# Performance work log

Hardware: AMD Instinct MI355X
Metric: run time of the kernel (lower is better)

The kernel has to match this reference:

```python
import jax, jax.numpy as jnp
import numpy as np

N_NODES = 100000
D = 128
N_EDGES = 640000


def _spmm(edge_index, w, x, n):
    # out[i] = sum over edges (i<-j): w * x[j]
    src, dst = edge_index[0], edge_index[1]
    return jax.ops.segment_sum(w[:, None] * x[dst], src, num_segments=n)


def setup_inputs() -> dict:
    key = jax.random.key(0)
    ks = jax.random.split(key, 8)
    inp = {
        "index_vectors": jax.random.normal(ks[0], (N_NODES, D), dtype=jnp.float32),
        "edge_index1": jax.random.randint(ks[1], (2, N_EDGES), 0, N_NODES, dtype=jnp.int64),
        "w1": jnp.ones((N_EDGES,), dtype=jnp.float32),
        "edge_index2": jax.random.randint(ks[2], (2, N_EDGES), 0, N_NODES, dtype=jnp.int64),
        "w2": jnp.ones((N_EDGES,), dtype=jnp.float32),
        "edge_index3": jax.random.randint(ks[3], (2, N_EDGES), 0, N_NODES, dtype=jnp.int64),
        "w3": jnp.ones((N_EDGES,), dtype=jnp.float32),
        "zeroth": jax.random.uniform(ks[4], (1, 1), dtype=jnp.float32),
        "fst": jax.random.uniform(ks[5], (1, 1), dtype=jnp.float32),
        "snd": jax.random.uniform(ks[6], (1, 1), dtype=jnp.float32),
        "trd": jax.random.uniform(ks[7], (1, 1), dtype=jnp.float32),
    }
    return inp


def reference(index_vectors, edge_index1, w1, edge_index2, w2, edge_index3, w3,
              zeroth, fst, snd, trd):
    n = index_vectors.shape[0]
    # hop-1 context: A @ x
    fst_ctx = _spmm(edge_index1, w1, index_vectors, n)
    # hop-2 context: A^2 @ roll(x, 1, axis=1)   (permute_vecs=True)
    snd_ctx = _spmm(edge_index2, w2, jnp.roll(index_vectors, 1, axis=1), n)
    # hop-3 context: A^3 @ roll(x, 2, axis=1)
    trd_ctx = _spmm(edge_index3, w3, jnp.roll(index_vectors, 2, axis=1), n)

    # relu-normalized scalar order weights (get_orders)
    r0, r1, r2, r3 = (jax.nn.relu(zeroth), jax.nn.relu(fst),
                      jax.nn.relu(snd), jax.nn.relu(trd))
    tot = r0 + r1 + r2 + r3 + 1e-6
    r0, r1, r2, r3 = r0 / tot, r1 / tot, r2 / tot, r3 / tot

    # use_sign=False -> plain weighted combination
    return r0 * index_vectors + r1 * fst_ctx + r2 * snd_ctx + r3 * trd_ctx
```

## Files before the change

kernel.cpp:

```cpp
#include <hip/hip_runtime.h>

#define N_NODES 100000
#define D 128
#define N_EDGES 640000
#define TOT_EDGES (3 * N_EDGES)

#define NB   256
#define NPB  391
#define BCAP 9216
#define OVF_CAP 16384
#define EPB  3072
#define BINA_BLOCKS (TOT_EDGES / EPB)
#define EPT  (EPB / 256)
#define NKEY 2048

#define WS_OVFCNT 0
#define WS_BCUR   64
#define WS_BBASE  16448
#define WS_BNUM   17472
#define WS_OVF    18496
#define WS_TMP    280640
#define WS_FREC   19155008
#define WS_OFFS   34515008
#define WS_XB     34915016
#define WS_TOTAL_FAST 60515016

#ifndef __has_builtin
#define __has_builtin(x) 0
#endif
#if __has_builtin(__builtin_amdgcn_alignbit)
#define ALIGN16(hi, lo) __builtin_amdgcn_alignbit((hi), (lo), 16)
#else
#define ALIGN16(hi, lo) (((hi) << 16) | ((lo) >> 16))
#endif

__device__ __forceinline__ void load_r(const float* z0, const float* z1,
                                       const float* z2, const float* z3,
                                       float& r0, float& r1, float& r2, float& r3) {
    r0 = fmaxf(z0[0], 0.0f);
    r1 = fmaxf(z1[0], 0.0f);
    r2 = fmaxf(z2[0], 0.0f);
    r3 = fmaxf(z3[0], 0.0f);
    float inv = 1.0f / (r0 + r1 + r2 + r3 + 1e-6f);
    r0 *= inv; r1 *= inv; r2 *= inv; r3 *= inv;
}

__device__ __forceinline__ unsigned short bf16rn(float f) {
    unsigned int u = __float_as_uint(f);
    u += 0x7FFFu + ((u >> 16) & 1u);
    return (unsigned short)(u >> 16);
}

__global__ void cast_kernel(const float* __restrict__ x, ushort* __restrict__ xb) {
    int i = blockIdx.x * 256 + threadIdx.x;
    if (i >= N_NODES * D / 4) return;
    float4 v = ((const float4*)x)[i];
    ushort4 h;
    h.x = bf16rn(v.x); h.y = bf16rn(v.y); h.z = bf16rn(v.z); h.w = bf16rn(v.w);
    ((ushort4*)xb)[i] = h;
}

__global__ void binA_kernel(const int* __restrict__ ei1, const float* __restrict__ w1,
                            const int* __restrict__ ei2, const float* __restrict__ w2,
                            const int* __restrict__ ei3, const float* __restrict__ w3,
                            const float* __restrict__ z0, const float* __restrict__ z1,
                            const float* __restrict__ z2, const float* __restrict__ z3,
                            int* __restrict__ bcur, int* __restrict__ ovf_count,
                            int4* __restrict__ ovf, int2* __restrict__ tmp) {
    __shared__ int hist[NB];
    __shared__ int base[NB];
    int t = threadIdx.x;
    hist[t] = 0;
    __syncthreads();

    float r0, r1, r2, r3;
    load_r(z0, z1, z2, z3, r0, r1, r2, r3);

    int e0 = blockIdx.x * EPB;
    int rank[EPT];
    int bkt[EPT];
    int rxv[EPT];
    float scv[EPT];

#pragma unroll
    for (int k = 0; k < EPT; ++k) {
        int e = e0 + t + k * 256;
        int set = e / N_EDGES;
        int idx = e - set * N_EDGES;
        const int* ei;  const float* w;  float rk;
        if      (set == 0) { ei = ei1; w = w1; rk = r1; }
        else if (set == 1) { ei = ei2; w = w2; rk = r2; }
        else               { ei = ei3; w = w3; rk = r3; }
        int src = ei[idx];
        int dst = ei[N_EDGES + idx];
        int b = src / NPB;
        int local = src - b * NPB;
        bkt[k]  = b;
        rxv[k]  = dst | (set << 17) | (local << 19);
        scv[k]  = rk * w[idx];
        rank[k] = atomicAdd(&hist[b], 1);
    }
    __syncthreads();

    {
        int h = hist[t];
        base[t] = h ? atomicAdd(&bcur[t * 16], h) : 0;
    }
    __syncthreads();

#pragma unroll
    for (int k = 0; k < EPT; ++k) {
        int b = bkt[k];
        int pos = base[b] + rank[k];
        if (pos < BCAP) {
            tmp[(size_t)b * BCAP + pos] = make_int2(rxv[k], __float_as_int(scv[k]));
        } else {
            int o = atomicAdd(ovf_count, 1);
            int src = b * NPB + ((rxv[k] >> 19) & 0x1FF);
            if (o < OVF_CAP) ovf[o] = make_int4(src, rxv[k] & 0x7FFFF,
                                                __float_as_int(scv[k]), 0);
        }
    }
}

__global__ void scanB_kernel(const int* __restrict__ bcur,
                             int* __restrict__ bbase, int* __restrict__ bnum,
                             int* __restrict__ offsets) {
    __shared__ int s[NB];
    int t = threadIdx.x;
    int n = bcur[t * 16];
    if (n > BCAP) n = BCAP;
    bnum[t] = n;
    s[t] = n;
    __syncthreads();
    for (int off = 1; off < NB; off <<= 1) {
        int v = (t >= off) ? s[t - off] : 0;
        __syncthreads();
        s[t] += v;
        __syncthreads();
    }
    bbase[t] = s[t] - n;
    if (t == NB - 1) offsets[N_NODES] = s[t];
}

__global__ void binB_kernel(const int2* __restrict__ tmp,
                            const int* __restrict__ bbase, const int* __restrict__ bnum,
                            int2* __restrict__ frecs, int* __restrict__ offsets) {
    __shared__ int d[NKEY];
    __shared__ int ts[256];
    __shared__ int cur[NKEY];
    int b = blockIdx.x;
    int t = threadIdx.x;
    int n = bnum[b];
    int gbase = bbase[b];

    for (int i = t; i < NKEY; i += 256) d[i] = 0;
    __syncthreads();
    for (int i = t; i < n; i += 256) {
        int rx = tmp[(size_t)b * BCAP + i].x;
        int key = (((rx >> 19) & 0x1FF) << 2) | ((rx >> 17) & 3);
        atomicAdd(&d[key], 1);
    }
    __syncthreads();

    int loc[8];
    int tot = 0;
#pragma unroll
    for (int k = 0; k < 8; ++k) { loc[k] = tot; tot += d[8 * t + k]; }
    ts[t] = tot;
    __syncthreads();
    for (int off = 1; off < 256; off <<= 1) {
        int v = (t >= off) ? ts[t - off] : 0;
        __syncthreads();
        ts[t] += v;
        __syncthreads();
    }
    int tbase = ts[t] - tot;
#pragma unroll
    for (int k = 0; k < 8; ++k) cur[8 * t + k] = tbase + loc[k];
    __syncthreads();

    int node0 = b * NPB;
    for (int l = t; l < NPB; l += 256) {
        int node = node0 + l;
        if (node < N_NODES) offsets[node] = gbase + cur[l << 2];
    }
    __syncthreads();

    for (int i = t; i < n; i += 256) {
        int2 rec = tmp[(size_t)b * BCAP + i];
        int key = (((rec.x >> 19) & 0x1FF) << 2) | ((rec.x >> 17) & 3);
        int pos = atomicAdd(&cur[key], 1);
        frecs[gbase + pos] = make_int2(rec.x & 0x7FFFF, rec.y);
    }
}

#define GB_ACCUM(RX, RY)                                                       \
    {                                                                          \
        const uint4* rowp = (const uint4*)(xb + (size_t)((RX) & 0x1FFFF) * D); \
        uint4 v = rowp[l16];                                                   \
        int sh = ((RX) >> 17) & 3;                                             \
        float sc = __int_as_float(RY);                                         \
        unsigned int pw = (unsigned int)__shfl((int)v.w, prevq);               \
        unsigned int s1x = ALIGN16(v.x, pw);                                   \
        unsigned int s1y = ALIGN16(v.y, v.x);                                  \
        unsigned int s1z = ALIGN16(v.z, v.y);                                  \
        unsigned int s1w = ALIGN16(v.w, v.z);                                  \
        unsigned int u0 = (sh == 0) ? v.x : (sh == 1) ? s1x : pw;              \
        unsigned int u1 = (sh == 0) ? v.y : (sh == 1) ? s1y : v.x;             \
        unsigned int u2 = (sh == 0) ? v.z : (sh == 1) ? s1z : v.y;             \
        unsigned int u3 = (sh == 0) ? v.w : (sh == 1) ? s1w : v.z;             \
        acc0 += sc * __uint_as_float(u0 << 16);                                \
        acc1 += sc * __uint_as_float(u0 & 0xFFFF0000u);                        \
        acc2 += sc * __uint_as_float(u1 << 16);                                \
        acc3 += sc * __uint_as_float(u1 & 0xFFFF0000u);                        \
        acc4 += sc * __uint_as_float(u2 << 16);                                \
        acc5 += sc * __uint_as_float(u2 & 0xFFFF0000u);                        \
        acc6 += sc * __uint_as_float(u3 << 16);                                \
        acc7 += sc * __uint_as_float(u3 & 0xFFFF0000u);                        \
    }

__global__ void gatherb_kernel(const float* __restrict__ x,
                               const ushort* __restrict__ xb,
                               const int* __restrict__ offsets,
                               const int2* __restrict__ recs,
                               const float* __restrict__ z0, const float* __restrict__ z1,
                               const float* __restrict__ z2, const float* __restrict__ z3,
                               float* __restrict__ out) {
    int wid  = (blockIdx.x * blockDim.x + threadIdx.x) >> 6;
    int lane = threadIdx.x & 63;
    if (wid >= N_NODES) return;

    float r0, r1, r2, r3;
    load_r(z0, z1, z2, z3, r0, r1, r2, r3);

    int qt    = lane >> 4;
    int l16   = lane & 15;
    int prevq = (qt << 4) | ((l16 + 15) & 15);

    int beg = offsets[wid];
    int end = offsets[wid + 1];
    int count = end - beg;
    int cnt64 = (count < 64) ? count : 64;

    int mrx = 0, mry = 0;
    if (lane < cnt64) { int2 rec = recs[beg + lane]; mrx = rec.x; mry = rec.y; }

    float acc0 = 0.f, acc1 = 0.f, acc2 = 0.f, acc3 = 0.f;
    float acc4 = 0.f, acc5 = 0.f, acc6 = 0.f, acc7 = 0.f;

    for (int j = 0; j < cnt64; j += 4) {
        int srcl = j + qt;
        int rx = __shfl(mrx, srcl);
        int ry = __shfl(mry, srcl);
        GB_ACCUM(rx, ry)
    }
    for (int q = 64; q < count; q += 4) {
        int qq = q + qt;
        int rx = 0, ry = 0;
        if (qq < count) { int2 rec = recs[beg + qq]; rx = rec.x; ry = rec.y; }
        GB_ACCUM(rx, ry)
    }

    acc0 += __shfl_xor(acc0, 16); acc0 += __shfl_xor(acc0, 32);
    acc1 += __shfl_xor(acc1, 16); acc1 += __shfl_xor(acc1, 32);
    acc2 += __shfl_xor(acc2, 16); acc2 += __shfl_xor(acc2, 32);
    acc3 += __shfl_xor(acc3, 16); acc3 += __shfl_xor(acc3, 32);
    acc4 += __shfl_xor(acc4, 16); acc4 += __shfl_xor(acc4, 32);
    acc5 += __shfl_xor(acc5, 16); acc5 += __shfl_xor(acc5, 32);
    acc6 += __shfl_xor(acc6, 16); acc6 += __shfl_xor(acc6, 32);
    acc7 += __shfl_xor(acc7, 16); acc7 += __shfl_xor(acc7, 32);

    if (lane < 16) {
        const float4* xr = (const float4*)(x + (size_t)wid * D);
        float4 xlo = xr[2 * l16];
        float4 xhi = xr[2 * l16 + 1];
        float4 olo, ohi;
        olo.x = r0 * xlo.x + acc0;
        olo.y = r0 * xlo.y + acc1;
        olo.z = r0 * xlo.z + acc2;
        olo.w = r0 * xlo.w + acc3;
        ohi.x = r0 * xhi.x + acc4;
        ohi.y = r0 * xhi.y + acc5;
        ohi.z = r0 * xhi.z + acc6;
        ohi.w = r0 * xhi.w + acc7;
        float4* op = (float4*)(out + (size_t)wid * D);
        op[2 * l16]     = olo;
        op[2 * l16 + 1] = ohi;
    }
}

__global__ void ovf_kernel(const float* __restrict__ x,
                           const int* __restrict__ ovf_count,
                           const int4* __restrict__ ovf,
                           float* __restrict__ out) {
    int total_waves = (gridDim.x * blockDim.x) >> 6;
    int gw   = (blockIdx.x * blockDim.x + threadIdx.x) >> 6;
    int lane = threadIdx.x & 63;
    int n = *ovf_count;
    if (n > OVF_CAP) n = OVF_CAP;
    for (int r = gw; r < n; r += total_waves) {
        int4 rec = ovf[r];
        int src = rec.x;
        int dst = rec.y & 0x1FFFF;
        int sh  = (rec.y >> 17) & 3;
        float sc = __int_as_float(rec.z);
        const float* xr = x + (size_t)dst * D;
        float* orow = out + (size_t)src * D;
        int c0 = 2 * lane, c1 = 2 * lane + 1;
        atomicAdd(&orow[c0], sc * xr[(c0 - sh) & 127]);
        atomicAdd(&orow[c1], sc * xr[(c1 - sh) & 127]);
    }
}

#define SCAN_BLOCKS ((N_NODES + 255) / 256)
#define WS_COUNTS   0
#define WS_OFFSETS  400000
#define WS_CURSORS  800008
#define WS_BSUM     1200008
#define WS_BPRE     1201576
#define WS_RECS     1203144
#define WS_NEEDED_MID (WS_RECS + (size_t)TOT_EDGES * 8)

__global__ void hist_kernel(const int* __restrict__ ei1, const int* __restrict__ ei2,
                            const int* __restrict__ ei3, int* __restrict__ counts) {
    int e = blockIdx.x * blockDim.x + threadIdx.x;
    if (e >= TOT_EDGES) return;
    int set = e / N_EDGES;
    int idx = e - set * N_EDGES;
    const int* ei = (set == 0) ? ei1 : (set == 1) ? ei2 : ei3;
    atomicAdd(&counts[ei[idx]], 1);
}

__global__ void scan1_kernel(const int* __restrict__ counts,
                             int* __restrict__ offsets, int* __restrict__ bsum) {
    __shared__ int s[256];
    int t = threadIdx.x;
    int i = blockIdx.x * 256 + t;
    int v = (i < N_NODES) ? counts[i] : 0;
    s[t] = v;
    __syncthreads();
    for (int off = 1; off < 256; off <<= 1) {
        int u = (t >= off) ? s[t - off] : 0;
        __syncthreads();
        s[t] += u;
        __syncthreads();
    }
    if (i < N_NODES) offsets[i] = s[t] - v;
    if (t == 255) bsum[blockIdx.x] = s[255];
}

__global__ void scan2_kernel(const int* __restrict__ bsum, int* __restrict__ bpre) {
    __shared__ int s[512];
    int t = threadIdx.x;
    int v = (t < SCAN_BLOCKS) ? bsum[t] : 0;
    s[t] = v;
    __syncthreads();
    for (int off = 1; off < 512; off <<= 1) {
        int u = (t >= off) ? s[t - off] : 0;
        __syncthreads();
        s[t] += u;
        __syncthreads();
    }
    if (t < SCAN_BLOCKS) bpre[t] = s[t] - v;
}

__global__ void scan3_kernel(int* __restrict__ offsets, const int* __restrict__ bpre,
                             int* __restrict__ cursors) {
    int i = blockIdx.x * 256 + threadIdx.x;
    if (i < N_NODES) {
        int v = offsets[i] + bpre[blockIdx.x];
        offsets[i] = v;
        cursors[i] = v;
    }
    if (i == 0) offsets[N_NODES] = TOT_EDGES;
}

__global__ void fill_kernel(const int* __restrict__ ei1, const float* __restrict__ w1,
                            const int* __restrict__ ei2, const float* __restrict__ w2,
                            const int* __restrict__ ei3, const float* __restrict__ w3,
                            const float* __restrict__ z0, const float* __restrict__ z1,
                            const float* __restrict__ z2, const float* __restrict__ z3,
                            int* __restrict__ cursors, int2* __restrict__ recs) {
    int e = blockIdx.x * blockDim.x + threadIdx.x;
    if (e >= TOT_EDGES) return;
    int set = e / N_EDGES;
    int idx = e - set * N_EDGES;
    const int* ei;  const float* w;
    if      (set == 0) { ei = ei1; w = w1; }
    else if (set == 1) { ei = ei2; w = w2; }
    else               { ei = ei3; w = w3; }
    float r0, r1, r2, r3;
    load_r(z0, z1, z2, z3, r0, r1, r2, r3);
    float rk = (set == 0) ? r1 : (set == 1) ? r2 : r3;
    int src = ei[idx];
    int dst = ei[N_EDGES + idx];
    float scale = rk * w[idx];
    int pos = atomicAdd(&cursors[src], 1);
    recs[pos] = make_int2(dst | (set << 17), __float_as_int(scale));
}

__global__ void gatherd_kernel(const float* __restrict__ x,
                               const int* __restrict__ offsets,
                               const int2* __restrict__ recs,
                               const float* __restrict__ z0, const float* __restrict__ z1,
                               const float* __restrict__ z2, const float* __restrict__ z3,
                               float* __restrict__ out) {
    int wid  = (blockIdx.x * blockDim.x + threadIdx.x) >> 6;
    int lane = threadIdx.x & 63;
    if (wid >= N_NODES) return;
    float r0, r1, r2, r3;
    load_r(z0, z1, z2, z3, r0, r1, r2, r3);
    float2 xv = ((const float2*)(x + (size_t)wid * D))[lane];
    int beg = offsets[wid];
    int end = offsets[wid + 1];
    float2 a0 = {0.f, 0.f}, a1 = {0.f, 0.f}, a2 = {0.f, 0.f};
    for (int j = beg; j < end; ++j) {
        int2 rec = recs[j];
        float2 v = ((const float2*)(x + (size_t)(rec.x & 0x1FFFF) * D))[lane];
        int sh = (rec.x >> 17) & 3;
        float sc = __int_as_float(rec.y);
        if      (sh == 0) { a0.x += sc * v.x; a0.y += sc * v.y; }
        else if (sh == 1) { a1.x += sc * v.x; a1.y += sc * v.y; }
        else               { a2.x += sc * v.x; a2.y += sc * v.y; }
    }
    int prev = (lane + 63) & 63;
    float r1y = __shfl(a1.y, prev);
    float r2x = __shfl(a2.x, prev);
    float r2y = __shfl(a2.y, prev);
    float2 o;
    o.x = r0 * xv.x + a0.x + r1y  + r2x;
    o.y = r0 * xv.y + a0.y + a1.x + r2y;
    ((float2*)(out + (size_t)wid * D))[lane] = o;
}

extern "C" void kernel_launch(void* const* d_in, const int* in_sizes, int n_in,
                              void* d_out, int out_size, void* d_ws, size_t ws_size,
                              hipStream_t stream) {
    const float* x   = (const float*)d_in[0];
    const int*   ei1 = (const int*)  d_in[1];
    const float* w1  = (const float*)d_in[2];
    const int*   ei2 = (const int*)  d_in[3];
    const float* w2  = (const float*)d_in[4];
    const int*   ei3 = (const int*)  d_in[5];
    const float* w3  = (const float*)d_in[6];
    const float* z0  = (const float*)d_in[7];
    const float* z1  = (const float*)d_in[8];
    const float* z2  = (const float*)d_in[9];
    const float* z3  = (const float*)d_in[10];
    float* out = (float*)d_out;
    char* wsc = (char*)d_ws;

    if (ws_size >= WS_TOTAL_FAST) {
        int*    ovf_count = (int*)   (wsc + WS_OVFCNT);
        int*    bcur      = (int*)   (wsc + WS_BCUR);
        int*    bbase     = (int*)   (wsc + WS_BBASE);
        int*    bnum      = (int*)   (wsc + WS_BNUM);
        int4*   ovf       = (int4*)  (wsc + WS_OVF);
        int2*   tmp       = (int2*)  (wsc + WS_TMP);
        int2*   frecs     = (int2*)  (wsc + WS_FREC);
        int*    offsets   = (int*)   (wsc + WS_OFFS);
        ushort* xb        = (ushort*)(wsc + WS_XB);

        hipMemsetAsync(wsc, 0, WS_BBASE, stream);
        cast_kernel<<<(N_NODES * D / 4 + 255) / 256, 256, 0, stream>>>(x, xb);
        binA_kernel<<<BINA_BLOCKS, 256, 0, stream>>>(ei1, w1, ei2, w2, ei3, w3,
                                                     z0, z1, z2, z3,
                                                     bcur, ovf_count, ovf, tmp);
        scanB_kernel<<<1, NB, 0, stream>>>(bcur, bbase, bnum, offsets);
        binB_kernel<<<NB, 256, 0, stream>>>(tmp, bbase, bnum, frecs, offsets);
        gatherb_kernel<<<(N_NODES * 64 + 255) / 256, 256, 0, stream>>>(x, xb, offsets,
                                                                       frecs, z0, z1, z2, z3,
                                                                       out);
        ovf_kernel<<<128, 256, 0, stream>>>(x, ovf_count, ovf, out);
    } else {
        int*  counts  = (int*) (wsc + WS_COUNTS);
        int*  offsets = (int*) (wsc + WS_OFFSETS);
        int*  cursors = (int*) (wsc + WS_CURSORS);
        int*  bsum    = (int*) (wsc + WS_BSUM);
        int*  bpre    = (int*) (wsc + WS_BPRE);
        int2* recs    = (int2*)(wsc + WS_RECS);

        hipMemsetAsync(counts, 0, N_NODES * sizeof(int), stream);
        hist_kernel<<<TOT_EDGES / 256, 256, 0, stream>>>(ei1, ei2, ei3, counts);
        scan1_kernel<<<SCAN_BLOCKS, 256, 0, stream>>>(counts, offsets, bsum);
        scan2_kernel<<<1, 512, 0, stream>>>(bsum, bpre);
        scan3_kernel<<<SCAN_BLOCKS, 256, 0, stream>>>(offsets, bpre, cursors);
        fill_kernel<<<TOT_EDGES / 256, 256, 0, stream>>>(ei1, w1, ei2, w2, ei3, w3,
                                                         z0, z1, z2, z3, cursors, recs);
        gatherd_kernel<<<(N_NODES * 64 + 255) / 256, 256, 0, stream>>>(x, offsets, recs,
                                                                       z0, z1, z2, z3, out);
    }
}
```

Measured before the change: 280.3 us.

## Restructure edge binning into deterministic hist/scan/place with in-place bucket sort

The two-level binning of edges by source node now uses 1024 smaller buckets. Bucket offsets come from a per-block histogram and a column scan instead of global atomics. Each block stages its records in shared memory sorted by bucket before writing them out, so global stores are grouped. The second pass keeps each bucket's records in registers and sorts them in place in tmp, dropping the separate frecs buffer and the global scan. Gather now reads per-node offset and count arrays. This aims to cut atomic contention, scattered writes and memory traffic, at the cost of an extra histogram pass over the edge indices and a serial column-scan kernel.

```diff
diff --git a/kernel.cpp b/kernel.cpp
--- a/kernel.cpp
+++ b/kernel.cpp
@@ -5,25 +5,29 @@
 #define N_EDGES 640000
 #define TOT_EDGES (3 * N_EDGES)
 
-#define NB   256
-#define NPB  391
-#define BCAP 9216
+#define NB   1024
+#define NPB  98
+#define BCAP 2304
+#define RPT  9
 #define OVF_CAP 16384
-#define EPB  3072
-#define BINA_BLOCKS (TOT_EDGES / EPB)
-#define EPT  (EPB / 256)
-#define NKEY 2048
+#define NKEY 512
+
+#define EPBA 2560
+#define SETBLKA (N_EDGES / EPBA)
+#define BLKA (3 * SETBLKA)
+#define EPT2 (EPBA / 256)
+
+#define CAST_BLOCKS ((N_NODES * D / 4 + 255) / 256)
 
 #define WS_OVFCNT 0
-#define WS_BCUR   64
-#define WS_BBASE  16448
-#define WS_BNUM   17472
-#define WS_OVF    18496
-#define WS_TMP    280640
-#define WS_FREC   19155008
-#define WS_OFFS   34515008
-#define WS_XB     34915016
-#define WS_TOTAL_FAST 60515016
+#define WS_CNT    64
+#define WS_TOT    3072064
+#define WS_OVF    3076160
+#define WS_TMP    3338304
+#define WS_OFFS   22212672
+#define WS_CNTS   22612672
+#define WS_XB     23012672
+#define WS_TOTAL_FAST 48612672
 
 #ifndef __has_builtin
 #define __has_builtin(x) 0
@@ -51,7 +55,8 @@
     return (unsigned short)(u >> 16);
 }
 
-__global__ void cast_kernel(const float* __restrict__ x, ushort* __restrict__ xb) {
+__global__ __launch_bounds__(256) void cast_kernel(const float* __restrict__ x,
+                                                   ushort* __restrict__ xb) {
     int i = blockIdx.x * 256 + threadIdx.x;
     if (i >= N_NODES * D / 4) return;
     float4 v = ((const float4*)x)[i];
@@ -60,113 +65,156 @@
     ((ushort4*)xb)[i] = h;
 }
 
-__global__ void binA_kernel(const int* __restrict__ ei1, const float* __restrict__ w1,
-                            const int* __restrict__ ei2, const float* __restrict__ w2,
-                            const int* __restrict__ ei3, const float* __restrict__ w3,
-                            const float* __restrict__ z0, const float* __restrict__ z1,
-                            const float* __restrict__ z2, const float* __restrict__ z3,
-                            int* __restrict__ bcur, int* __restrict__ ovf_count,
-                            int4* __restrict__ ovf, int2* __restrict__ tmp) {
-    __shared__ int hist[NB];
-    __shared__ int base[NB];
+__global__ __launch_bounds__(256) void histA_kernel(
+        const int* __restrict__ ei1, const int* __restrict__ ei2,
+        const int* __restrict__ ei3, int* __restrict__ counts) {
+    __shared__ int h[NB];
     int t = threadIdx.x;
-    hist[t] = 0;
-    __syncthreads();
-
+    int blk = blockIdx.x;
+    for (int i = t; i < NB; i += 256) h[i] = 0;
+    __syncthreads();
+    int set = blk / SETBLKA;
+    int e0  = (blk - set * SETBLKA) * EPBA;
+    const int* ei = (set == 0) ? ei1 : (set == 1) ? ei2 : ei3;
+    for (int i = t; i < EPBA; i += 256) {
+        atomicAdd(&h[ei[e0 + i] / NPB], 1);
+    }
+    __syncthreads();
+    for (int i = t; i < NB; i += 256) counts[blk * NB + i] = h[i];
+}
+
+__global__ __launch_bounds__(256) void scanA_kernel(int* __restrict__ counts,
+                                                    int* __restrict__ totals) {
+    int b = blockIdx.x * 256 + threadIdx.x;
+    int run = 0;
+    for (int blk = 0; blk < BLKA; ++blk) {
+        int c = counts[blk * NB + b];
+        counts[blk * NB + b] = run;
+        run += c;
+    }
+    totals[b] = run;
+}
+
+__global__ __launch_bounds__(256) void placeA_kernel(
+        const int* __restrict__ ei1, const float* __restrict__ w1,
+        const int* __restrict__ ei2, const float* __restrict__ w2,
+        const int* __restrict__ ei3, const float* __restrict__ w3,
+        const float* __restrict__ z0, const float* __restrict__ z1,
+        const float* __restrict__ z2, const float* __restrict__ z3,
+        const int* __restrict__ bbase,
+        int* __restrict__ ovf_count, int4* __restrict__ ovf,
+        int2* __restrict__ tmp) {
+    __shared__ int bb[NB];
+    __shared__ int h[NB];
+    __shared__ int ts[256];
+    __shared__ int2 srec[EPBA];
+    __shared__ int gx[EPBA];
+
+    int t = threadIdx.x;
+    int blk = blockIdx.x;
+    for (int i = t; i < NB; i += 256) { bb[i] = bbase[blk * NB + i]; h[i] = 0; }
+    __syncthreads();
+
+    int set = blk / SETBLKA;
+    int e0  = (blk - set * SETBLKA) * EPBA;
+    const int* ei;  const float* w;  float rk;
     float r0, r1, r2, r3;
     load_r(z0, z1, z2, z3, r0, r1, r2, r3);
-
-    int e0 = blockIdx.x * EPB;
-    int rank[EPT];
-    int bkt[EPT];
-    int rxv[EPT];
-    float scv[EPT];
-
-#pragma unroll
-    for (int k = 0; k < EPT; ++k) {
-        int e = e0 + t + k * 256;
-        int set = e / N_EDGES;
-        int idx = e - set * N_EDGES;
-        const int* ei;  const float* w;  float rk;
-        if      (set == 0) { ei = ei1; w = w1; rk = r1; }
-        else if (set == 1) { ei = ei2; w = w2; rk = r2; }
-        else               { ei = ei3; w = w3; rk = r3; }
+    if      (set == 0) { ei = ei1; w = w1; rk = r1; }
+    else if (set == 1) { ei = ei2; w = w2; rk = r2; }
+    else               { ei = ei3; w = w3; rk = r3; }
+
+    int bkt[EPT2], rnk[EPT2], lcl[EPT2], dstv[EPT2];
+    float scv[EPT2];
+#pragma unroll
+    for (int k = 0; k < EPT2; ++k) {
+        int idx = e0 + t + k * 256;
         int src = ei[idx];
-        int dst = ei[N_EDGES + idx];
+        dstv[k] = ei[N_EDGES + idx];
+        scv[k]  = rk * w[idx];
         int b = src / NPB;
-        int local = src - b * NPB;
-        bkt[k]  = b;
-        rxv[k]  = dst | (set << 17) | (local << 19);
-        scv[k]  = rk * w[idx];
-        rank[k] = atomicAdd(&hist[b], 1);
-    }
-    __syncthreads();
-
-    {
-        int h = hist[t];
-        base[t] = h ? atomicAdd(&bcur[t * 16], h) : 0;
-    }
-    __syncthreads();
-
-#pragma unroll
-    for (int k = 0; k < EPT; ++k) {
+        bkt[k] = b;
+        lcl[k] = src - b * NPB;
+        rnk[k] = atomicAdd(&h[b], 1);
+    }
+    __syncthreads();
+
+    int loc[4];
+    int tot = 0;
+#pragma unroll
+    for (int k = 0; k < 4; ++k) { loc[k] = tot; tot += h[4 * t + k]; }
+    ts[t] = tot;
+    __syncthreads();
+    for (int off = 1; off < 256; off <<= 1) {
+        int v = (t >= off) ? ts[t - off] : 0;
+        __syncthreads();
+        ts[t] += v;
+        __syncthreads();
+    }
+    int tb = ts[t] - tot;
+    __syncthreads();
+#pragma unroll
+    for (int k = 0; k < 4; ++k) h[4 * t + k] = tb + loc[k];
+    __syncthreads();
+
+#pragma unroll
+    for (int k = 0; k < EPT2; ++k) {
         int b = bkt[k];
-        int pos = base[b] + rank[k];
-        if (pos < BCAP) {
-            tmp[(size_t)b * BCAP + pos] = make_int2(rxv[k], __float_as_int(scv[k]));
+        int s = h[b] + rnk[k];
+        int rx = dstv[k] | (set << 17) | (lcl[k] << 19);
+        srec[s] = make_int2(rx, __float_as_int(scv[k]));
+        int p = bb[b] + rnk[k];
+        if (p < BCAP) {
+            gx[s] = b * BCAP + p;
         } else {
+            gx[s] = -1;
             int o = atomicAdd(ovf_count, 1);
-            int src = b * NPB + ((rxv[k] >> 19) & 0x1FF);
-            if (o < OVF_CAP) ovf[o] = make_int4(src, rxv[k] & 0x7FFFF,
-                                                __float_as_int(scv[k]), 0);
+            if (o < OVF_CAP) ovf[o] = make_int4(b * NPB + lcl[k],
+                                               dstv[k] | (set << 17),
+                                               __float_as_int(scv[k]), 0);
         }
     }
-}
-
-__global__ void scanB_kernel(const int* __restrict__ bcur,
-                             int* __restrict__ bbase, int* __restrict__ bnum,
-                             int* __restrict__ offsets) {
-    __shared__ int s[NB];
-    int t = threadIdx.x;
-    int n = bcur[t * 16];
-    if (n > BCAP) n = BCAP;
-    bnum[t] = n;
-    s[t] = n;
-    __syncthreads();
-    for (int off = 1; off < NB; off <<= 1) {
-        int v = (t >= off) ? s[t - off] : 0;
-        __syncthreads();
-        s[t] += v;
-        __syncthreads();
-    }
-    bbase[t] = s[t] - n;
-    if (t == NB - 1) offsets[N_NODES] = s[t];
-}
-
-__global__ void binB_kernel(const int2* __restrict__ tmp,
-                            const int* __restrict__ bbase, const int* __restrict__ bnum,
-                            int2* __restrict__ frecs, int* __restrict__ offsets) {
-    __shared__ int d[NKEY];
+    __syncthreads();
+
+    for (int s = t; s < EPBA; s += 256) {
+        int g = gx[s];
+        if (g >= 0) tmp[g] = srec[s];
+    }
+}
+
+__global__ __launch_bounds__(256) void binB_kernel(
+        const int* __restrict__ totals, int2* __restrict__ tmp,
+        int* __restrict__ offs, int* __restrict__ cnts) {
+    __shared__ int dH[NKEY];
     __shared__ int ts[256];
     __shared__ int cur[NKEY];
+    __shared__ int nb[NPB + 1];
     int b = blockIdx.x;
     int t = threadIdx.x;
-    int n = bnum[b];
-    int gbase = bbase[b];
-
-    for (int i = t; i < NKEY; i += 256) d[i] = 0;
-    __syncthreads();
-    for (int i = t; i < n; i += 256) {
-        int rx = tmp[(size_t)b * BCAP + i].x;
-        int key = (((rx >> 19) & 0x1FF) << 2) | ((rx >> 17) & 3);
-        atomicAdd(&d[key], 1);
-    }
-    __syncthreads();
-
-    int loc[8];
-    int tot = 0;
-#pragma unroll
-    for (int k = 0; k < 8; ++k) { loc[k] = tot; tot += d[8 * t + k]; }
+    int n = totals[b];
+    if (n > BCAP) n = BCAP;
+
+    int mrx[RPT], mry[RPT];
+#pragma unroll
+    for (int k = 0; k < RPT; ++k) {
+        int i = t + k * 256;
+        if (i < n) { int2 r = tmp[(size_t)b * BCAP + i]; mrx[k] = r.x; mry[k] = r.y; }
+        else       { mrx[k] = -1; mry[k] = 0; }
+    }
+
+    dH[t] = 0; dH[t + 256] = 0;
+    __syncthreads();
+#pragma unroll
+    for (int k = 0; k < RPT; ++k) {
+        if (mrx[k] != -1) {
+            int key = (((mrx[k] >> 19) & 0x7F) << 2) | ((mrx[k] >> 17) & 3);
+            atomicAdd(&dH[key], 1);
+        }
+    }
+    __syncthreads();
+
+    int k0 = dH[2 * t], k1 = dH[2 * t + 1];
+    int tot = k0 + k1;
     ts[t] = tot;
     __syncthreads();
     for (int off = 1; off < 256; off <<= 1) {
@@ -175,23 +223,29 @@
         ts[t] += v;
         __syncthreads();
     }
-    int tbase = ts[t] - tot;
-#pragma unroll
-    for (int k = 0; k < 8; ++k) cur[8 * t + k] = tbase + loc[k];
-    __syncthreads();
-
-    int node0 = b * NPB;
-    for (int l = t; l < NPB; l += 256) {
-        int node = node0 + l;
-        if (node < N_NODES) offsets[node] = gbase + cur[l << 2];
-    }
-    __syncthreads();
-
-    for (int i = t; i < n; i += 256) {
-        int2 rec = tmp[(size_t)b * BCAP + i];
-        int key = (((rec.x >> 19) & 0x1FF) << 2) | ((rec.x >> 17) & 3);
-        int pos = atomicAdd(&cur[key], 1);
-        frecs[gbase + pos] = make_int2(rec.x & 0x7FFFF, rec.y);
+    int tb = ts[t] - tot;
+    cur[2 * t]     = tb;
+    cur[2 * t + 1] = tb + k0;
+    __syncthreads();
+
+    if (t <= NPB) nb[t] = (t < NPB) ? cur[t << 2] : n;
+    __syncthreads();
+
+#pragma unroll
+    for (int k = 0; k < RPT; ++k) {
+        if (mrx[k] != -1) {
+            int key = (((mrx[k] >> 19) & 0x7F) << 2) | ((mrx[k] >> 17) & 3);
+            int pos = atomicAdd(&cur[key], 1);
+            tmp[(size_t)b * BCAP + pos] = make_int2(mrx[k], mry[k]);
+        }
+    }
+
+    if (t < NPB) {
+        int node = b * NPB + t;
+        if (node < N_NODES) {
+            offs[node] = b * BCAP + nb[t];
+            cnts[node] = nb[t + 1] - nb[t];
+        }
     }
 }
 
@@ -220,13 +274,13 @@
         acc7 += sc * __uint_as_float(u3 & 0xFFFF0000u);                        \
     }
 
-__global__ void gatherb_kernel(const float* __restrict__ x,
-                               const ushort* __restrict__ xb,
-                               const int* __restrict__ offsets,
-                               const int2* __restrict__ recs,
-                               const float* __restrict__ z0, const float* __restrict__ z1,
-                               const float* __restrict__ z2, const float* __restrict__ z3,
-                               float* __restrict__ out) {
+__global__ __launch_bounds__(256) void gatherb_kernel(
+        const float* __restrict__ x, const ushort* __restrict__ xb,
+        const int* __restrict__ offs, const int* __restrict__ cnts,
+        const int2* __restrict__ recs,
+        const float* __restrict__ z0, const float* __restrict__ z1,
+        const float* __restrict__ z2, const float* __restrict__ z3,
+        float* __restrict__ out) {
     int wid  = (blockIdx.x * blockDim.x + threadIdx.x) >> 6;
     int lane = threadIdx.x & 63;
     if (wid >= N_NODES) return;
@@ -238,9 +292,8 @@
     int l16   = lane & 15;
     int prevq = (qt << 4) | ((l16 + 15) & 15);
 
-    int beg = offsets[wid];
-    int end = offsets[wid + 1];
-    int count = end - beg;
+    int beg   = offs[wid];
+    int count = cnts[wid];
     int cnt64 = (count < 64) ? count : 64;
 
     int mrx = 0, mry = 0;
@@ -453,25 +506,24 @@
 
     if (ws_size >= WS_TOTAL_FAST) {
         int*    ovf_count = (int*)   (wsc + WS_OVFCNT);
-        int*    bcur      = (int*)   (wsc + WS_BCUR);
-        int*    bbase     = (int*)   (wsc + WS_BBASE);
-        int*    bnum      = (int*)   (wsc + WS_BNUM);
+        int*    counts    = (int*)   (wsc + WS_CNT);
+        int*    totals    = (int*)   (wsc + WS_TOT);
         int4*   ovf       = (int4*)  (wsc + WS_OVF);
         int2*   tmp       = (int2*)  (wsc + WS_TMP);
-        int2*   frecs     = (int2*)  (wsc + WS_FREC);
-        int*    offsets   = (int*)   (wsc + WS_OFFS);
+        int*    offs      = (int*)   (wsc + WS_OFFS);
+        int*    cnts      = (int*)   (wsc + WS_CNTS);
         ushort* xb        = (ushort*)(wsc + WS_XB);
 
-        hipMemsetAsync(wsc, 0, WS_BBASE, stream);
-        cast_kernel<<<(N_NODES * D / 4 + 255) / 256, 256, 0, stream>>>(x, xb);
-        binA_kernel<<<BINA_BLOCKS, 256, 0, stream>>>(ei1, w1, ei2, w2, ei3, w3,
-                                                     z0, z1, z2, z3,
-                                                     bcur, ovf_count, ovf, tmp);
-        scanB_kernel<<<1, NB, 0, stream>>>(bcur, bbase, bnum, offsets);
-        binB_kernel<<<NB, 256, 0, stream>>>(tmp, bbase, bnum, frecs, offsets);
-        gatherb_kernel<<<(N_NODES * 64 + 255) / 256, 256, 0, stream>>>(x, xb, offsets,
-                                                                       frecs, z0, z1, z2, z3,
-                                                                       out);
+        hipMemsetAsync(wsc, 0, 64, stream);
+        cast_kernel<<<CAST_BLOCKS, 256, 0, stream>>>(x, xb);
+        histA_kernel<<<BLKA, 256, 0, stream>>>(ei1, ei2, ei3, counts);
+        scanA_kernel<<<4, 256, 0, stream>>>(counts, totals);
+        placeA_kernel<<<BLKA, 256, 0, stream>>>(ei1, w1, ei2, w2, ei3, w3,
+                                                z0, z1, z2, z3,
+                                                counts, ovf_count, ovf, tmp);
+        binB_kernel<<<NB, 256, 0, stream>>>(totals, tmp, offs, cnts);
+        gatherb_kernel<<<(N_NODES * 64 + 255) / 256, 256, 0, stream>>>(
+            x, xb, offs, cnts, tmp, z0, z1, z2, z3, out);
         ovf_kernel<<<128, 256, 0, stream>>>(x, ovf_count, ovf, out);
     } else {
         int*  counts  = (int*) (wsc + WS_COUNTS);
```

After: 296.6 us. +5.8%, slower.
